# Optimization experiments

Hardware: AMD Instinct MI355X
Metric: run time of the kernel (lower is better)

The kernel has to match this reference:

```python
import jax, jax.numpy as jnp
import numpy as np

EPS = 1e-5

def _ln(x, g, b):
    m = jnp.mean(x, axis=-1, keepdims=True)
    v = jnp.var(x, axis=-1, keepdims=True)
    return (x - m) / jnp.sqrt(v + EPS) * g + b

def _partition(x, nw):
    b, h, w, c = x.shape
    x = x.reshape(b, nw, h // nw, nw, w // nw, c).transpose(0, 1, 3, 2, 4, 5)
    return x.reshape(b * nw * nw, h // nw, w // nw, c)

def _merge(x, nw):
    b_, h, w, c = x.shape
    b = b_ // (nw * nw)
    x = x.reshape(b, nw, nw, h, w, c).transpose(0, 1, 3, 2, 4, 5)
    return x.reshape(b, nw * h, nw * w, c)

def _window_attn(q, k, v, width, height, nw, mask):
    b, _, c = q.shape
    q = q.reshape(b, height, width, c)
    k = k.reshape(b, height, width, c)
    v = v.reshape(b, height, width, c)
    sh, sw = (height // nw) // 2, (width // nw) // 2
    q = jnp.roll(q, (-sh, -sw), (1, 2))
    k = jnp.roll(k, (-sh, -sw), (1, 2))
    v = jnp.roll(v, (-sh, -sw), (1, 2))
    q = _partition(q, nw); k = _partition(k, nw); v = _partition(v, nw)
    N = (height // nw) * (width // nw)
    b_ = b * nw * nw
    qf = q.reshape(b_, N, c); kf = k.reshape(b_, N, c); vf = v.reshape(b_, N, c)
    scale = jnp.asarray(c, qf.dtype) ** 0.5
    scores = jnp.einsum('bnc,bmc->bnm', qf, kf) / scale  # [b_, N, N]
    scores = (scores.reshape(b, nw * nw, N, N) + mask[None]).reshape(b_, N, N)
    attn = jax.nn.softmax(scores, axis=-1)
    out = jnp.einsum('bnm,bmc->bnc', attn, vf)
    out = _merge(out.reshape(b_, height // nw, width // nw, c), nw)
    out = jnp.roll(out, (sh, sw), (1, 2))
    return out.reshape(b, height * width, c)

def _block(feat0, feat1, width, height, mask, nw, wq, wk, wv, wfc, g, be, ffn=None):
    q = feat0 @ wq; k = feat1 @ wk; v = feat1 @ wv
    a = _window_attn(q, k, v, width, height, nw, mask)
    a = _ln(a @ wfc, g, be)
    if ffn is not None:
        w1, w2, fg, fb = ffn
        h = jax.nn.gelu(jnp.concatenate([feat0, a], axis=-1) @ w1, approximate=False)
        a = _ln(h @ w2, fg, fb)
    return feat0 + a

def setup_inputs() -> dict:
    key = jax.random.key(0)
    B, H, W, NW, D = 8, 128, 128, 8, 256
    N = (H // NW) * (W // NW)
    ks = jax.random.split(key, 16)
    s = D ** -0.5
    return {
        'feat0': jax.random.normal(ks[0], (B, H * W, D), jnp.float32),
        'feat1': jax.random.normal(ks[1], (B, H * W, D), jnp.float32),
        'mask_attn': jax.random.normal(ks[2], (NW * NW, N, N), jnp.float32),
        'width': W, 'height': H, 'n_window': NW,
        'intra_wq': jax.random.normal(ks[3], (D, D), jnp.float32) * s,
        'intra_wk': jax.random.normal(ks[4], (D, D), jnp.float32) * s,
        'intra_wv': jax.random.normal(ks[5], (D, D), jnp.float32) * s,
        'intra_wfc': jax.random.normal(ks[6], (D, D), jnp.float32) * s,
        'intra_g': jnp.ones((D,), jnp.float32),
        'intra_b': jnp.zeros((D,), jnp.float32),
        'inter_wq': jax.random.normal(ks[7], (D, D), jnp.float32) * s,
        'inter_wk': jax.random.normal(ks[8], (D, D), jnp.float32) * s,
        'inter_wv': jax.random.normal(ks[9], (D, D), jnp.float32) * s,
        'inter_wfc': jax.random.normal(ks[10], (D, D), jnp.float32) * s,
        'inter_g': jnp.ones((D,), jnp.float32),
        'inter_b': jnp.zeros((D,), jnp.float32),
        'inter_w1': jax.random.normal(ks[11], (2 * D, 2 * D * 4), jnp.float32) * (2 * D) ** -0.5,
        'inter_w2': jax.random.normal(ks[12], (2 * D * 4, D), jnp.float32) * (2 * D * 4) ** -0.5,
        'inter_fg': jnp.ones((D,), jnp.float32),
        'inter_fb': jnp.zeros((D,), jnp.float32),
    }

def reference(feat0, feat1, mask_attn, width, height, n_window,
              intra_wq, intra_wk, intra_wv, intra_wfc, intra_g, intra_b,
              inter_wq, inter_wk, inter_wv, inter_wfc, inter_g, inter_b,
              inter_w1, inter_w2, inter_fg, inter_fb):
    f0 = _block(feat0, feat0, width, height, mask_attn, n_window,
                intra_wq, intra_wk, intra_wv, intra_wfc, intra_g, intra_b)
    out = _block(f0, feat1, width, height, mask_attn, n_window,
                 inter_wq, inter_wk, inter_wv, inter_wfc, inter_g, inter_b,
                 ffn=(inter_w1, inter_w2, inter_fg, inter_fb))
    return out
```

## Files before the change

### kernel.cpp

```cpp
#include <hip/hip_runtime.h>

typedef unsigned short u16;
typedef unsigned int   u32;

using f32x4  = __attribute__((ext_vector_type(4))) float;
using bf16x8 = __attribute__((ext_vector_type(8))) __bf16;

__device__ inline u16 f2bf(float f) {
  return __builtin_bit_cast(u16, (__bf16)f);
}
__device__ inline float bf2f(u16 v) {
  u32 u = ((u32)v) << 16;
  return __builtin_bit_cast(float, u);
}

__device__ inline void gl_lds16(const u16* g, u16* l) {
  __builtin_amdgcn_global_load_lds((const __attribute__((address_space(1))) void*)g,
                                   (__attribute__((address_space(3))) void*)l,
                                   16, 0, 0);
}

__device__ inline int perm_fwd(int m) {
  int b = m >> 14, rem = m & 16383;
  int h = rem >> 7, w = rem & 127;
  int hr = (h - 8) & 127, wr = (w - 8) & 127;
  int win = (b << 6) | ((hr >> 4) << 3) | (wr >> 4);
  return (win << 8) | ((hr & 15) << 4) | (wr & 15);
}
__device__ inline int perm_inv(int r) {
  int win = r >> 8, t = r & 255;
  int b = win >> 6, wy = (win >> 3) & 7, wx = win & 7;
  int h = (((wy << 4) | (t >> 4)) + 8) & 127;
  int w = (((wx << 4) | (t & 15)) + 8) & 127;
  return (b << 14) | (h << 7) | w;
}


enum { MODE_QKV = 0, MODE_SCORES = 1, MODE_PV = 2, MODE_F32 = 3, MODE_FFN1 = 4 };

template<int MODE>
__global__ __launch_bounds__(256)
void gemm_nt(const u16* __restrict__ A, int lda, long long sAz,
             const u16* __restrict__ Bt, int ldb, long long sBz,
             u16* __restrict__ OutB, float* __restrict__ OutF,
             const float* __restrict__ mask, int K, int ldo)
{
  __shared__ __align__(16) u16 sA[128 * 64];
  __shared__ __align__(16) u16 sB[128 * 64];

  const int tid  = threadIdx.x;
  const int lane = tid & 63;
  const int wave = tid >> 6;
  const int l15  = lane & 15;
  const int quad = lane >> 4;
  const int wm   = (wave >> 1) << 6;
  const int wn   = (wave & 1) << 6;

  const int nbx = (int)gridDim.x, nby = (int)gridDim.y;
  const int nwg = nbx * nby * (int)gridDim.z;
  const int bid0 = (int)blockIdx.x + nbx * ((int)blockIdx.y + nby * (int)blockIdx.z);
  const int work = (bid0 & 7) * (nwg >> 3) + (bid0 >> 3);
  const int bx  = work % nbx;
  const int tm  = work / nbx;
  const int by  = tm % nby;
  const int z   = tm / nby;
  const int m0  = by << 7;
  const int n0  = bx << 7;

  const u16* Ab = A  + (long long)z * sAz;
  const u16* Bb = Bt + (long long)z * sBz;

  const int cd = ((lane & 7) ^ ((lane >> 3) & 7)) << 3;
  const int rs = (wave << 5) + (lane >> 3);
  const u16* ga0 = Ab + (long long)(m0 + rs) * lda + cd;
  const u16* gb0 = Bb + (long long)(n0 + rs) * ldb + cd;
  u16* la0 = &sA[wave << 11];
  u16* lb0 = &sB[wave << 11];

  const f32x4 zero = {0.f, 0.f, 0.f, 0.f};
  f32x4 acc[4][4];
#pragma unroll
  for (int i = 0; i < 4; ++i)
#pragma unroll
    for (int j = 0; j < 4; ++j) acc[i][j] = zero;

  for (int k0 = 0; k0 < K; k0 += 64) {
    __syncthreads();
#pragma unroll
    for (int p = 0; p < 4; ++p) {
      gl_lds16(ga0 + k0 + (p << 3) * lda, la0 + (p << 9));
      gl_lds16(gb0 + k0 + (p << 3) * ldb, lb0 + (p << 9));
    }
    __syncthreads();
#pragma unroll
    for (int kk = 0; kk < 2; ++kk) {
      const int sw = (((quad | (kk << 2)) ^ (l15 & 7)) << 3);
      bf16x8 af[4], bfr[4];
#pragma unroll
      for (int i = 0; i < 4; ++i) {
        af[i]  = *(const bf16x8*)(sA + ((wm + (i << 4) + l15) << 6) + sw);
        bfr[i] = *(const bf16x8*)(sB + ((wn + (i << 4) + l15) << 6) + sw);
      }
#pragma unroll
      for (int i = 0; i < 4; ++i)
#pragma unroll
        for (int j = 0; j < 4; ++j)
          acc[i][j] = __builtin_amdgcn_mfma_f32_16x16x32_bf16(af[i], bfr[j], acc[i][j], 0, 0, 0);
    }
  }

#pragma unroll
  for (int i = 0; i < 4; ++i) {
#pragma unroll
    for (int r = 0; r < 4; ++r) {
      int mg = m0 + wm + (i << 4) + (quad << 2) + r;
      if constexpr (MODE == MODE_QKV) {
        u16* orow = OutB + ((long long)perm_fwd(mg) << 8);
#pragma unroll
        for (int j = 0; j < 4; ++j) {
          int ng = n0 + wn + (j << 4) + l15;
          orow[ng] = f2bf(acc[i][j][r]);
        }
      } else if constexpr (MODE == MODE_SCORES) {
        const float* mrow = mask + (((long long)(z & 63)) << 16) + ((long long)mg << 8);
        u16* orow = OutB + (((long long)z) << 16) + ((long long)mg << 8);
#pragma unroll
        for (int j = 0; j < 4; ++j) {
          int ng = n0 + wn + (j << 4) + l15;
          orow[ng] = f2bf(acc[i][j][r] * 0.0625f + mrow[ng]);
        }
      } else if constexpr (MODE == MODE_PV) {
        u16* orow = OutB + ((long long)perm_inv((z << 8) + mg) << 8);
#pragma unroll
        for (int j = 0; j < 4; ++j) {
          int ng = n0 + wn + (j << 4) + l15;
          orow[ng] = f2bf(acc[i][j][r]);
        }
      } else if constexpr (MODE == MODE_F32) {
        float* orow = OutF + ((long long)mg << 8);
#pragma unroll
        for (int j = 0; j < 4; ++j) {
          int ng = n0 + wn + (j << 4) + l15;
          orow[ng] = acc[i][j][r];
        }
      } else {
        u16* orow = OutB + (long long)mg * ldo;
#pragma unroll
        for (int j = 0; j < 4; ++j) {
          int ng = n0 + wn + (j << 4) + l15;
          float v = acc[i][j][r];
          float t = v * fmaf(v * v, -0.071354816f, -1.5957691216f);
          float g = v * __builtin_amdgcn_rcpf(1.0f + __expf(t));
          orow[ng] = f2bf(g);
        }
      }
    }
  }
}

__global__ __launch_bounds__(256)
void scores_softmax(const u16* __restrict__ Q, const u16* __restrict__ Kw,
                    const float* __restrict__ mask, u16* __restrict__ SP)
{
  __shared__ __align__(16) u16 sA[128 * 64];
  __shared__ __align__(16) u16 sB[256 * 64];

  const int tid  = threadIdx.x;
  const int lane = tid & 63;
  const int wave = tid >> 6;
  const int l15  = lane & 15;
  const int quad = lane >> 4;

  const int nwg  = (int)(gridDim.x * gridDim.y);
  const int bid0 = (int)blockIdx.x + (int)gridDim.x * (int)blockIdx.y;
  const int work = (bid0 & 7) * (nwg >> 3) + (bid0 >> 3);
  const int mhalf = work & 1;
  const int z     = work >> 1;
  const int m0    = mhalf << 7;

  const u16* Ab = Q  + ((long long)z << 16);
  const u16* Bb = Kw + ((long long)z << 16);

  const int cd  = ((lane & 7) ^ ((lane >> 3) & 7)) << 3;
  const int rsA = (wave << 5) + (lane >> 3);
  const int rsB = (wave << 6) + (lane >> 3);
  const u16* ga0 = Ab + (long long)(m0 + rsA) * 256 + cd;
  const u16* gb0 = Bb + (long long)rsB * 256 + cd;
  u16* la0 = &sA[wave << 11];
  u16* lb0 = &sB[wave << 12];

  const f32x4 zero = {0.f, 0.f, 0.f, 0.f};
  f32x4 acc[2][16];
#pragma unroll
  for (int i = 0; i < 2; ++i)
#pragma unroll
    for (int j = 0; j < 16; ++j) acc[i][j] = zero;

  for (int k0 = 0; k0 < 256; k0 += 64) {
    __syncthreads();
#pragma unroll
    for (int p = 0; p < 4; ++p)
      gl_lds16(ga0 + k0 + (p << 3) * 256, la0 + (p << 9));
#pragma unroll
    for (int p = 0; p < 8; ++p)
      gl_lds16(gb0 + k0 + (p << 3) * 256, lb0 + (p << 9));
    __syncthreads();
#pragma unroll
    for (int kk = 0; kk < 2; ++kk) {
      const int sw = (((quad | (kk << 2)) ^ (l15 & 7)) << 3);
      bf16x8 af0 = *(const bf16x8*)(sA + (((wave << 5) + l15) << 6) + sw);
      bf16x8 af1 = *(const bf16x8*)(sA + (((wave << 5) + 16 + l15) << 6) + sw);
#pragma unroll
      for (int j = 0; j < 16; ++j) {
        bf16x8 bf = *(const bf16x8*)(sB + (((j << 4) + l15) << 6) + sw);
        acc[0][j] = __builtin_amdgcn_mfma_f32_16x16x32_bf16(af0, bf, acc[0][j], 0, 0, 0);
        acc[1][j] = __builtin_amdgcn_mfma_f32_16x16x32_bf16(af1, bf, acc[1][j], 0, 0, 0);
      }
    }
  }

  const float* mbase = mask + (((long long)(z & 63)) << 16);
#pragma unroll
  for (int i = 0; i < 2; ++i) {
#pragma unroll
    for (int r = 0; r < 4; ++r) {
      const int mg = m0 + (wave << 5) + (i << 4) + (quad << 2) + r;
      const float* mrow = mbase + ((long long)mg << 8);
      float sv[16];
      float mx = -3.0e38f;
#pragma unroll
      for (int j = 0; j < 16; ++j) {
        sv[j] = acc[i][j][r] * 0.0625f + mrow[(j << 4) + l15];
        mx = fmaxf(mx, sv[j]);
      }
#pragma unroll
      for (int o = 1; o < 16; o <<= 1) mx = fmaxf(mx, __shfl_xor(mx, o));
      float sum = 0.f;
#pragma unroll
      for (int j = 0; j < 16; ++j) { sv[j] = __expf(sv[j] - mx); sum += sv[j]; }
#pragma unroll
      for (int o = 1; o < 16; o <<= 1) sum += __shfl_xor(sum, o);
      const float inv = 1.0f / sum;
      u16* orow = SP + (((long long)z) << 16) + ((long long)mg << 8);
#pragma unroll
      for (int j = 0; j < 16; ++j) orow[(j << 4) + l15] = f2bf(sv[j] * inv);
    }
  }
}

__global__ __launch_bounds__(256)
void transpose256(const u16* __restrict__ src, u16* __restrict__ dst)
{
  __shared__ u16 t[32][33];
  const int z  = blockIdx.z;
  const int tx = blockIdx.x << 5;
  const int ty = blockIdx.y << 5;
  const int c  = threadIdx.x & 31;
  const int r0 = threadIdx.x >> 5;
  const long long base = ((long long)z) << 16;
#pragma unroll
  for (int p = 0; p < 4; ++p) {
    int r = r0 + (p << 3);
    t[r][c] = src[base + (long long)(ty + r) * 256 + tx + c];
  }
  __syncthreads();
#pragma unroll
  for (int p = 0; p < 4; ++p) {
    int r = r0 + (p << 3);
    dst[base + (long long)(tx + r) * 256 + ty + c] = t[c][r];
  }
}

template<int MODE>
__global__ __launch_bounds__(256)
void ln_kernel(const float* __restrict__ Y, const float* __restrict__ G,
               const float* __restrict__ Bb, const float* __restrict__ ResF,
               const u16* __restrict__ ResB,
               float* __restrict__ OutF, u16* __restrict__ OutB)
{
  const int row  = (blockIdx.x << 2) + (threadIdx.x >> 6);
  const int lane = threadIdx.x & 63;
  float4 x = *((const float4*)(Y + ((long long)row << 8)) + lane);
  float s  = x.x + x.y + x.z + x.w;
  float s2 = x.x * x.x + x.y * x.y + x.z * x.z + x.w * x.w;
#pragma unroll
  for (int o = 32; o > 0; o >>= 1) { s += __shfl_xor(s, o); s2 += __shfl_xor(s2, o); }
  float mean = s * (1.0f / 256.0f);
  float var  = s2 * (1.0f / 256.0f) - mean * mean;
  float rstd = rsqrtf(var + 1e-5f);
  float4 g = *((const float4*)G + lane);
  float4 b = *((const float4*)Bb + lane);
  float v0 = (x.x - mean) * rstd * g.x + b.x;
  float v1 = (x.y - mean) * rstd * g.y + b.y;
  float v2 = (x.z - mean) * rstd * g.z + b.z;
  float v3 = (x.w - mean) * rstd * g.w + b.w;
  if constexpr (MODE == 0) {
    float4 rr = *((const float4*)(ResF + ((long long)row << 8)) + lane);
    ushort4 ub;
    ub.x = f2bf(v0 + rr.x); ub.y = f2bf(v1 + rr.y);
    ub.z = f2bf(v2 + rr.z); ub.w = f2bf(v3 + rr.w);
    *((ushort4*)(OutB + ((long long)row << 9)) + lane) = ub;
  } else if constexpr (MODE == 1) {
    ushort4 ub; ub.x = f2bf(v0); ub.y = f2bf(v1); ub.z = f2bf(v2); ub.w = f2bf(v3);
    *((ushort4*)(OutB + ((long long)row << 9) + 256) + lane) = ub;
  } else {
    ushort4 rb = *((const ushort4*)(ResB + ((long long)row << 9)) + lane);
    float4 o;
    o.x = v0 + bf2f(rb.x); o.y = v1 + bf2f(rb.y);
    o.z = v2 + bf2f(rb.z); o.w = v3 + bf2f(rb.w);
    *((float4*)(OutF + ((long long)row << 8)) + lane) = o;
  }
}

__global__ __launch_bounds__(256)
void cvt_f32_bf16(const float* __restrict__ src, u16* __restrict__ dst, int n4)
{
  int i = blockIdx.x * 256 + threadIdx.x;
  if (i >= n4) return;
  float4 v = ((const float4*)src)[i];
  ushort4 u; u.x = f2bf(v.x); u.y = f2bf(v.y); u.z = f2bf(v.z); u.w = f2bf(v.w);
  ((ushort4*)dst)[i] = u;
}

__global__ __launch_bounds__(256)
void wtrans(const float* __restrict__ src, u16* __restrict__ dst, int R, int C)
{
  int idx = blockIdx.x * 256 + threadIdx.x;
  if (idx >= R * C) return;
  int r = idx / C, c = idx - r * C;
  dst[c * R + r] = f2bf(src[idx]);
}

extern "C" void kernel_launch(void* const* d_in, const int* in_sizes, int n_in,
                              void* d_out, int out_size, void* d_ws, size_t ws_size,
                              hipStream_t stream)
{
  (void)in_sizes; (void)n_in; (void)out_size;
  const float* feat0 = (const float*)d_in[0];
  const float* feat1 = (const float*)d_in[1];
  const float* mask  = (const float*)d_in[2];
  const float* wq1 = (const float*)d_in[6];
  const float* wk1 = (const float*)d_in[7];
  const float* wv1 = (const float*)d_in[8];
  const float* wf1 = (const float*)d_in[9];
  const float* g1  = (const float*)d_in[10];
  const float* b1  = (const float*)d_in[11];
  const float* wq2 = (const float*)d_in[12];
  const float* wk2 = (const float*)d_in[13];
  const float* wv2 = (const float*)d_in[14];
  const float* wf2 = (const float*)d_in[15];
  const float* g2  = (const float*)d_in[16];
  const float* b2  = (const float*)d_in[17];
  const float* w1  = (const float*)d_in[18];
  const float* w2  = (const float*)d_in[19];
  const float* fg  = (const float*)d_in[20];
  const float* fb  = (const float*)d_in[21];

  const size_t Mi = 1048576;
  const size_t WB = 4 * Mi;
  const int Mtot = 131072;

  int nc = 8;
  for (int c = 1; c <= 8; c <<= 1) {
    size_t S = (size_t)(Mtot / c) * 512;
    if (7 * S + WB <= ws_size) { nc = c; break; }
  }
  const int Mc = Mtot / nc;
  const size_t S = (size_t)Mc * 512;

  char* ws = (char*)d_ws;
  u16*   featb = (u16*)(ws);
  u16*   SPb   = featb;
  u16*   qw    = (u16*)(ws + S);
  u16*   Ob    = qw;
  u16*   hbuf  = featb;
  u16*   kw    = (u16*)(ws + 2 * S);
  u16*   vw    = (u16*)(ws + 3 * S);
  float* y     = (float*)(ws + 2 * S);
  u16*   vt    = (u16*)(ws + 4 * S);
  u16*   xcat  = (u16*)(ws + 5 * S);
  u16*   wb    = (u16*)(ws + 7 * S);
  u16* wq1t = wb;            u16* wk1t = wb + 65536;  u16* wv1t = wb + 131072; u16* wf1t = wb + 196608;
  u16* wq2t = wb + 262144;   u16* wk2t = wb + 327680; u16* wv2t = wb + 393216; u16* wf2t = wb + 458752;
  u16* w1t  = wb + 524288;
  u16* w2t  = wb + 524288 + 1048576;

  const dim3 blk(256);
  const dim3 gBig(2, Mc / 128, 1);
  const int  Wc = Mc / 256;
  const dim3 gWin(2, 2, Wc);
  const dim3 gSS(2, Wc);
  const dim3 gTr(8, 8, Wc);
  const int  gRows = Mc / 4;
  const int  MF = Mc / 4;
  const dim3 gF1(16, MF / 128, 1);
  const dim3 gF2(2, MF / 128, 1);
  const int  gRowsF = MF / 4;

  wtrans<<<256, blk, 0, stream>>>(wq1, wq1t, 256, 256);
  wtrans<<<256, blk, 0, stream>>>(wk1, wk1t, 256, 256);
  wtrans<<<256, blk, 0, stream>>>(wv1, wv1t, 256, 256);
  wtrans<<<256, blk, 0, stream>>>(wf1, wf1t, 256, 256);
  wtrans<<<256, blk, 0, stream>>>(wq2, wq2t, 256, 256);
  wtrans<<<256, blk, 0, stream>>>(wk2, wk2t, 256, 256);
  wtrans<<<256, blk, 0, stream>>>(wv2, wv2t, 256, 256);
  wtrans<<<256, blk, 0, stream>>>(wf2, wf2t, 256, 256);
  wtrans<<<4096, blk, 0, stream>>>(w1, w1t, 512, 2048);
  wtrans<<<2048, blk, 0, stream>>>(w2, w2t, 2048, 256);

  for (int c = 0; c < nc; ++c) {
    const long long off = (long long)c * Mc * 256;
    const float* f0in = feat0 + off;
    const float* f1in = feat1 + off;
    float* outp = (float*)d_out + off;

    cvt_f32_bf16<<<gRows, blk, 0, stream>>>(f0in, featb, Mc * 64);
    gemm_nt<MODE_QKV><<<gBig, blk, 0, stream>>>(featb, 256, 0, wq1t, 256, 0, qw, nullptr, nullptr, 256, 0);
    gemm_nt<MODE_QKV><<<gBig, blk, 0, stream>>>(featb, 256, 0, wk1t, 256, 0, kw, nullptr, nullptr, 256, 0);
    gemm_nt<MODE_QKV><<<gBig, blk, 0, stream>>>(featb, 256, 0, wv1t, 256, 0, vw, nullptr, nullptr, 256, 0);
    transpose256<<<gTr, blk, 0, stream>>>(vw, vt);
    scores_softmax<<<gSS, blk, 0, stream>>>(qw, kw, mask, SPb);
    gemm_nt<MODE_PV><<<gWin, blk, 0, stream>>>(SPb, 256, 65536, vt, 256, 65536, Ob, nullptr, nullptr, 256, 0);
    gemm_nt<MODE_F32><<<gBig, blk, 0, stream>>>(Ob, 256, 0, wf1t, 256, 0, nullptr, y, nullptr, 256, 0);
    ln_kernel<0><<<gRows, blk, 0, stream>>>(y, g1, b1, f0in, nullptr, nullptr, xcat);

    cvt_f32_bf16<<<gRows, blk, 0, stream>>>(f1in, featb, Mc * 64);
    gemm_nt<MODE_QKV><<<gBig, blk, 0, stream>>>(xcat, 512, 0, wq2t, 256, 0, qw, nullptr, nullptr, 256, 0);
    gemm_nt<MODE_QKV><<<gBig, blk, 0, stream>>>(featb, 256, 0, wk2t, 256, 0, kw, nullptr, nullptr, 256, 0);
    gemm_nt<MODE_QKV><<<gBig, blk, 0, stream>>>(featb, 256, 0, wv2t, 256, 0, vw, nullptr, nullptr, 256, 0);
    transpose256<<<gTr, blk, 0, stream>>>(vw, vt);
    scores_softmax<<<gSS, blk, 0, stream>>>(qw, kw, mask, SPb);
    gemm_nt<MODE_PV><<<gWin, blk, 0, stream>>>(SPb, 256, 65536, vt, 256, 65536, Ob, nullptr, nullptr, 256, 0);
    gemm_nt<MODE_F32><<<gBig, blk, 0, stream>>>(Ob, 256, 0, wf2t, 256, 0, nullptr, y, nullptr, 256, 0);
    ln_kernel<1><<<gRows, blk, 0, stream>>>(y, g2, b2, nullptr, nullptr, nullptr, xcat);

    for (int mc = 0; mc < 4; ++mc) {
      const u16* xc = xcat + (long long)mc * MF * 512;
      gemm_nt<MODE_FFN1><<<gF1, blk, 0, stream>>>(xc, 512, 0, w1t, 512, 0,
                                                  hbuf, nullptr, nullptr, 512, 2048);
      gemm_nt<MODE_F32><<<gF2, blk, 0, stream>>>(hbuf, 2048, 0, w2t, 2048, 0,
                                                 nullptr, y, nullptr, 2048, 0);
      ln_kernel<2><<<gRowsF, blk, 0, stream>>>(y, fg, fb, nullptr,
                                               xcat + (long long)mc * MF * 512,
                                               outp + (long long)mc * MF * 256, nullptr);
    }
  }
}
```

Before: 1.800 ms.

## Fuse output projection GEMMs with LayerNorm epilogue and drop block swizzle

Adds a gemm_ln kernel that computes a full 256-wide output row tile (64 rows x 256 cols) per block and applies LayerNorm, residual add and output conversion in the epilogue. This replaces the three GEMM-to-f32 plus separate ln_kernel pairs and removes the f32 intermediate round trip through memory. It also removes the XCD-aware block index remapping in gemm_nt and scores_softmax in favour of direct blockIdx mapping. In exchange the fused kernel uses smaller M tiles with no double buffering, so there are fewer blocks for the K=2048 FFN2 GEMM, and the plain block mapping may hurt L2 locality.

```diff
diff --git a/kernel.cpp b/kernel.cpp
--- a/kernel.cpp
+++ b/kernel.cpp
@@ -55,17 +55,9 @@
   const int quad = lane >> 4;
   const int wm   = (wave >> 1) << 6;
   const int wn   = (wave & 1) << 6;
-
-  const int nbx = (int)gridDim.x, nby = (int)gridDim.y;
-  const int nwg = nbx * nby * (int)gridDim.z;
-  const int bid0 = (int)blockIdx.x + nbx * ((int)blockIdx.y + nby * (int)blockIdx.z);
-  const int work = (bid0 & 7) * (nwg >> 3) + (bid0 >> 3);
-  const int bx  = work % nbx;
-  const int tm  = work / nbx;
-  const int by  = tm % nby;
-  const int z   = tm / nby;
-  const int m0  = by << 7;
-  const int n0  = bx << 7;
+  const int z    = blockIdx.z;
+  const int m0   = (int)(blockIdx.y) << 7;
+  const int n0   = (int)(blockIdx.x) << 7;
 
   const u16* Ab = A  + (long long)z * sAz;
   const u16* Bb = Bt + (long long)z * sBz;
@@ -120,14 +112,6 @@
         for (int j = 0; j < 4; ++j) {
           int ng = n0 + wn + (j << 4) + l15;
           orow[ng] = f2bf(acc[i][j][r]);
-        }
-      } else if constexpr (MODE == MODE_SCORES) {
-        const float* mrow = mask + (((long long)(z & 63)) << 16) + ((long long)mg << 8);
-        u16* orow = OutB + (((long long)z) << 16) + ((long long)mg << 8);
-#pragma unroll
-        for (int j = 0; j < 4; ++j) {
-          int ng = n0 + wn + (j << 4) + l15;
-          orow[ng] = f2bf(acc[i][j][r] * 0.0625f + mrow[ng]);
         }
       } else if constexpr (MODE == MODE_PV) {
         u16* orow = OutB + ((long long)perm_inv((z << 8) + mg) << 8);
@@ -171,11 +155,8 @@
   const int l15  = lane & 15;
   const int quad = lane >> 4;
 
-  const int nwg  = (int)(gridDim.x * gridDim.y);
-  const int bid0 = (int)blockIdx.x + (int)gridDim.x * (int)blockIdx.y;
-  const int work = (bid0 & 7) * (nwg >> 3) + (bid0 >> 3);
-  const int mhalf = work & 1;
-  const int z     = work >> 1;
+  const int mhalf = (int)blockIdx.x;
+  const int z     = (int)blockIdx.y;
   const int m0    = mhalf << 7;
 
   const u16* Ab = Q  + ((long long)z << 16);
@@ -248,6 +229,108 @@
   }
 }
 
+enum { LN_XCAT0 = 0, LN_XCAT1 = 1, LN_OUT = 2 };
+
+template<int MODE>
+__global__ __launch_bounds__(256)
+void gemm_ln(const u16* __restrict__ A, int lda,
+             const u16* __restrict__ Bt,
+             const float* __restrict__ G, const float* __restrict__ Bias,
+             const float* __restrict__ ResF, const u16* __restrict__ ResB,
+             float* __restrict__ OutF, u16* __restrict__ OutB, int K)
+{
+  __shared__ __align__(16) u16 sA[64 * 64];
+  __shared__ __align__(16) u16 sB[256 * 64];
+
+  const int tid  = threadIdx.x;
+  const int lane = tid & 63;
+  const int wave = tid >> 6;
+  const int l15  = lane & 15;
+  const int quad = lane >> 4;
+  const int m0   = (int)blockIdx.x << 6;
+
+  const int cd  = ((lane & 7) ^ ((lane >> 3) & 7)) << 3;
+  const int rsA = (wave << 4) + (lane >> 3);
+  const int rsB = (wave << 6) + (lane >> 3);
+  const u16* ga0 = A  + (long long)(m0 + rsA) * lda + cd;
+  const u16* gb0 = Bt + (long long)rsB * K + cd;
+  u16* la0 = &sA[wave << 10];
+  u16* lb0 = &sB[wave << 12];
+
+  const f32x4 zero = {0.f, 0.f, 0.f, 0.f};
+  f32x4 acc[16];
+#pragma unroll
+  for (int j = 0; j < 16; ++j) acc[j] = zero;
+
+  for (int k0 = 0; k0 < K; k0 += 64) {
+    __syncthreads();
+#pragma unroll
+    for (int p = 0; p < 2; ++p)
+      gl_lds16(ga0 + k0 + (p << 3) * lda, la0 + (p << 9));
+#pragma unroll
+    for (int p = 0; p < 8; ++p)
+      gl_lds16(gb0 + k0 + (p << 3) * K, lb0 + (p << 9));
+    __syncthreads();
+#pragma unroll
+    for (int kk = 0; kk < 2; ++kk) {
+      const int sw = (((quad | (kk << 2)) ^ (l15 & 7)) << 3);
+      bf16x8 af = *(const bf16x8*)(sA + (((wave << 4) + l15) << 6) + sw);
+#pragma unroll
+      for (int j = 0; j < 16; ++j) {
+        bf16x8 bf = *(const bf16x8*)(sB + (((j << 4) + l15) << 6) + sw);
+        acc[j] = __builtin_amdgcn_mfma_f32_16x16x32_bf16(af, bf, acc[j], 0, 0, 0);
+      }
+    }
+  }
+
+  float gj[16], bj[16];
+#pragma unroll
+  for (int j = 0; j < 16; ++j) {
+    gj[j] = G[(j << 4) + l15];
+    bj[j] = Bias[(j << 4) + l15];
+  }
+
+#pragma unroll
+  for (int r = 0; r < 4; ++r) {
+    const int mg = m0 + (wave << 4) + (quad << 2) + r;
+    float s = 0.f, s2 = 0.f;
+#pragma unroll
+    for (int j = 0; j < 16; ++j) {
+      float v = acc[j][r];
+      s += v; s2 += v * v;
+    }
+#pragma unroll
+    for (int o = 1; o < 16; o <<= 1) { s += __shfl_xor(s, o); s2 += __shfl_xor(s2, o); }
+    const float mean = s * (1.0f / 256.0f);
+    const float var  = s2 * (1.0f / 256.0f) - mean * mean;
+    const float rstd = rsqrtf(var + 1e-5f);
+    if constexpr (MODE == LN_XCAT0) {
+      u16* orow = OutB + ((long long)mg << 9);
+      const float* rrow = ResF + ((long long)mg << 8);
+#pragma unroll
+      for (int j = 0; j < 16; ++j) {
+        float v = (acc[j][r] - mean) * rstd * gj[j] + bj[j];
+        orow[(j << 4) + l15] = f2bf(v + rrow[(j << 4) + l15]);
+      }
+    } else if constexpr (MODE == LN_XCAT1) {
+      u16* orow = OutB + ((long long)mg << 9) + 256;
+#pragma unroll
+      for (int j = 0; j < 16; ++j) {
+        float v = (acc[j][r] - mean) * rstd * gj[j] + bj[j];
+        orow[(j << 4) + l15] = f2bf(v);
+      }
+    } else {
+      const u16* rrow = ResB + ((long long)mg << 9);
+      float* orow = OutF + ((long long)mg << 8);
+#pragma unroll
+      for (int j = 0; j < 16; ++j) {
+        float v = (acc[j][r] - mean) * rstd * gj[j] + bj[j];
+        orow[(j << 4) + l15] = v + bf2f(rrow[(j << 4) + l15]);
+      }
+    }
+  }
+}
+
 __global__ __launch_bounds__(256)
 void transpose256(const u16* __restrict__ src, u16* __restrict__ dst)
 {
@@ -268,47 +351,6 @@
   for (int p = 0; p < 4; ++p) {
     int r = r0 + (p << 3);
     dst[base + (long long)(tx + r) * 256 + ty + c] = t[c][r];
-  }
-}
-
-template<int MODE>
-__global__ __launch_bounds__(256)
-void ln_kernel(const float* __restrict__ Y, const float* __restrict__ G,
-               const float* __restrict__ Bb, const float* __restrict__ ResF,
-               const u16* __restrict__ ResB,
-               float* __restrict__ OutF, u16* __restrict__ OutB)
-{
-  const int row  = (blockIdx.x << 2) + (threadIdx.x >> 6);
-  const int lane = threadIdx.x & 63;
-  float4 x = *((const float4*)(Y + ((long long)row << 8)) + lane);
-  float s  = x.x + x.y + x.z + x.w;
-  float s2 = x.x * x.x + x.y * x.y + x.z * x.z + x.w * x.w;
-#pragma unroll
-  for (int o = 32; o > 0; o >>= 1) { s += __shfl_xor(s, o); s2 += __shfl_xor(s2, o); }
-  float mean = s * (1.0f / 256.0f);
-  float var  = s2 * (1.0f / 256.0f) - mean * mean;
-  float rstd = rsqrtf(var + 1e-5f);
-  float4 g = *((const float4*)G + lane);
-  float4 b = *((const float4*)Bb + lane);
-  float v0 = (x.x - mean) * rstd * g.x + b.x;
-  float v1 = (x.y - mean) * rstd * g.y + b.y;
-  float v2 = (x.z - mean) * rstd * g.z + b.z;
-  float v3 = (x.w - mean) * rstd * g.w + b.w;
-  if constexpr (MODE == 0) {
-    float4 rr = *((const float4*)(ResF + ((long long)row << 8)) + lane);
-    ushort4 ub;
-    ub.x = f2bf(v0 + rr.x); ub.y = f2bf(v1 + rr.y);
-    ub.z = f2bf(v2 + rr.z); ub.w = f2bf(v3 + rr.w);
-    *((ushort4*)(OutB + ((long long)row << 9)) + lane) = ub;
-  } else if constexpr (MODE == 1) {
-    ushort4 ub; ub.x = f2bf(v0); ub.y = f2bf(v1); ub.z = f2bf(v2); ub.w = f2bf(v3);
-    *((ushort4*)(OutB + ((long long)row << 9) + 256) + lane) = ub;
-  } else {
-    ushort4 rb = *((const ushort4*)(ResB + ((long long)row << 9)) + lane);
-    float4 o;
-    o.x = v0 + bf2f(rb.x); o.y = v1 + bf2f(rb.y);
-    o.z = v2 + bf2f(rb.z); o.w = v3 + bf2f(rb.w);
-    *((float4*)(OutF + ((long long)row << 8)) + lane) = o;
   }
 }
 
@@ -376,7 +418,6 @@
   u16*   hbuf  = featb;
   u16*   kw    = (u16*)(ws + 2 * S);
   u16*   vw    = (u16*)(ws + 3 * S);
-  float* y     = (float*)(ws + 2 * S);
   u16*   vt    = (u16*)(ws + 4 * S);
   u16*   xcat  = (u16*)(ws + 5 * S);
   u16*   wb    = (u16*)(ws + 7 * S);
@@ -392,10 +433,10 @@
   const dim3 gSS(2, Wc);
   const dim3 gTr(8, 8, Wc);
   const int  gRows = Mc / 4;
+  const int  gLN   = Mc / 64;
   const int  MF = Mc / 4;
   const dim3 gF1(16, MF / 128, 1);
-  const dim3 gF2(2, MF / 128, 1);
-  const int  gRowsF = MF / 4;
+  const int  gLNF  = MF / 64;
 
   wtrans<<<256, blk, 0, stream>>>(wq1, wq1t, 256, 256);
   wtrans<<<256, blk, 0, stream>>>(wk1, wk1t, 256, 256);
@@ -421,8 +462,7 @@
     transpose256<<<gTr, blk, 0, stream>>>(vw, vt);
     scores_softmax<<<gSS, blk, 0, stream>>>(qw, kw, mask, SPb);
     gemm_nt<MODE_PV><<<gWin, blk, 0, stream>>>(SPb, 256, 65536, vt, 256, 65536, Ob, nullptr, nullptr, 256, 0);
-    gemm_nt<MODE_F32><<<gBig, blk, 0, stream>>>(Ob, 256, 0, wf1t, 256, 0, nullptr, y, nullptr, 256, 0);
-    ln_kernel<0><<<gRows, blk, 0, stream>>>(y, g1, b1, f0in, nullptr, nullptr, xcat);
+    gemm_ln<LN_XCAT0><<<gLN, blk, 0, stream>>>(Ob, 256, wf1t, g1, b1, f0in, nullptr, nullptr, xcat, 256);
 
     cvt_f32_bf16<<<gRows, blk, 0, stream>>>(f1in, featb, Mc * 64);
     gemm_nt<MODE_QKV><<<gBig, blk, 0, stream>>>(xcat, 512, 0, wq2t, 256, 0, qw, nullptr, nullptr, 256, 0);
@@ -431,18 +471,15 @@
     transpose256<<<gTr, blk, 0, stream>>>(vw, vt);
     scores_softmax<<<gSS, blk, 0, stream>>>(qw, kw, mask, SPb);
     gemm_nt<MODE_PV><<<gWin, blk, 0, stream>>>(SPb, 256, 65536, vt, 256, 65536, Ob, nullptr, nullptr, 256, 0);
-    gemm_nt<MODE_F32><<<gBig, blk, 0, stream>>>(Ob, 256, 0, wf2t, 256, 0, nullptr, y, nullptr, 256, 0);
-    ln_kernel<1><<<gRows, blk, 0, stream>>>(y, g2, b2, nullptr, nullptr, nullptr, xcat);
+    gemm_ln<LN_XCAT1><<<gLN, blk, 0, stream>>>(Ob, 256, wf2t, g2, b2, nullptr, nullptr, nullptr, xcat, 256);
 
     for (int mc = 0; mc < 4; ++mc) {
       const u16* xc = xcat + (long long)mc * MF * 512;
       gemm_nt<MODE_FFN1><<<gF1, blk, 0, stream>>>(xc, 512, 0, w1t, 512, 0,
                                                   hbuf, nullptr, nullptr, 512, 2048);
-      gemm_nt<MODE_F32><<<gF2, blk, 0, stream>>>(hbuf, 2048, 0, w2t, 2048, 0,
-                                                 nullptr, y, nullptr, 2048, 0);
-      ln_kernel<2><<<gRowsF, blk, 0, stream>>>(y, fg, fb, nullptr,
-                                               xcat + (long long)mc * MF * 512,
-                                               outp + (long long)mc * MF * 256, nullptr);
-    }
-  }
-}
+      gemm_ln<LN_OUT><<<gLNF, blk, 0, stream>>>(hbuf, 2048, w2t, fg, fb, nullptr,
+                                                xcat + (long long)mc * MF * 512,
+                                                outp + (long long)mc * MF * 256, nullptr, 2048);
+    }
+  }
+}
```

After: 1.680 ms. 6.7% less time.
